# Optimization experiments

Hardware: AMD Instinct MI355X
Metric: run time of the kernel (lower is better)

## Reference

```python
import jax, jax.numpy as jnp
import numpy as np

D_MODEL = 2048
D_INNER = 4096
D_XB = 1024
D_STATE = 16
D_CONV = 4
DT_RANK = 128
BATCH = 2
SEQLEN = 2048
N_XB_HEAD = D_XB // D_STATE      # 64
N_C_HEAD = D_INNER // D_STATE    # 256
REP = N_C_HEAD // N_XB_HEAD      # 4
P = D_INNER // N_C_HEAD          # channels per head = 16


def setup_inputs() -> dict:
    key = jax.random.key(0)
    ks = jax.random.split(key, 8)
    rnd = lambda k, shape, sc: (jax.random.normal(k, shape, dtype=jnp.float32) * sc)
    hidden_states = jax.random.normal(ks[0], (BATCH, SEQLEN, D_MODEL), dtype=jnp.float32)
    in_proj_w = rnd(ks[1], (2 * D_XB + 2 * D_INNER, D_MODEL), 0.02)
    dt_in_proj_w = rnd(ks[2], (DT_RANK, D_MODEL), 0.02)
    lim = DT_RANK ** -0.5
    dt_proj_w = jax.random.uniform(ks[3], (D_INNER, DT_RANK), minval=-lim, maxval=lim, dtype=jnp.float32)
    # dt bias init: inverse-softplus of dt sampled log-uniform in [dt_min, dt_max]
    dt = jnp.exp(jax.random.uniform(ks[4], (D_INNER,), dtype=jnp.float32)
                 * (np.log(0.1) - np.log(0.001)) + np.log(0.001))
    dt = jnp.clip(dt, 1e-4, None)
    dt_proj_b = dt + jnp.log(-jnp.expm1(-dt))
    conv_w = rnd(ks[5], (D_INNER, 1, D_CONV), 0.2)
    conv_b = rnd(ks[6], (D_INNER,), 0.1)
    # A = -exp(A_log), A_log = log(arange(1..d_state)) per channel (S4D-real init)
    A_log = jnp.log(jnp.tile(jnp.arange(1, D_STATE + 1, dtype=jnp.float32), (D_INNER, 1)))
    D = jnp.ones((D_INNER,), dtype=jnp.float32)
    out_proj_w = rnd(ks[7], (D_MODEL, D_INNER), 0.02)
    return {"hidden_states": hidden_states, "in_proj_w": in_proj_w,
            "dt_in_proj_w": dt_in_proj_w, "dt_proj_w": dt_proj_w, "dt_proj_b": dt_proj_b,
            "conv_w": conv_w, "conv_b": conv_b, "A_log": A_log, "D": D,
            "out_proj_w": out_proj_w}


def reference(hidden_states, in_proj_w, dt_in_proj_w, dt_proj_w, dt_proj_b,
              conv_w, conv_b, A_log, D, out_proj_w):
    b, l, _ = hidden_states.shape
    h, p, n = N_C_HEAD, P, D_STATE
    A = -jnp.exp(A_log)                                   # (d_inner, n)
    A_h = A.reshape(h, p, n)

    zxbc = hidden_states @ in_proj_w.T                    # (b, l, 2*d_inner + 2*d_xb)
    z, x, Bm, Cm = jnp.split(zxbc, [D_INNER, D_INNER + D_XB, D_INNER + 2 * D_XB], axis=-1)

    # repeat_kv (GQA-style head repeat) on x and B before conv
    xh = jnp.repeat(x.reshape(b, l, N_XB_HEAD, D_STATE), REP, axis=2)   # (b, l, h, dstate)
    Bh = jnp.repeat(Bm.reshape(b, l, N_XB_HEAD, n), REP, axis=2)        # (b, l, h, n)
    Ch = Cm.reshape(b, l, h, n)                                         # (b, l, h, n)

    # causal depthwise conv1d + SiLU over d_inner channels
    u = xh.reshape(b, l, D_INNER).transpose(0, 2, 1)      # (b, d_inner, l)
    u = jnp.pad(u, ((0, 0), (0, 0), (D_CONV - 1, 0)))
    u = jax.lax.conv_general_dilated(u, conv_w, (1,), 'VALID',
                                     dimension_numbers=('NCH', 'OIH', 'NCH'),
                                     feature_group_count=D_INNER)
    u = jax.nn.silu(u + conv_b[None, :, None])            # (b, d_inner, l)
    u_bld = u.transpose(0, 2, 1)                          # (b, l, d_inner)

    # dt = softplus(dt_proj(dt_in_proj(h)) + dt_bias)
    dt = jax.nn.softplus((hidden_states @ dt_in_proj_w.T) @ dt_proj_w.T + dt_proj_b)  # (b, l, d_inner)

    dt_h = dt.reshape(b, l, h, p).transpose(1, 0, 2, 3)   # (l, b, h, p)
    u_h = u_bld.reshape(b, l, h, p).transpose(1, 0, 2, 3)
    B_l = Bh.transpose(1, 0, 2, 3)                        # (l, b, h, n)
    C_l = Ch.transpose(1, 0, 2, 3)

    def step(s, inp):
        dt_t, u_t, B_t, C_t = inp                         # (b,h,p),(b,h,p),(b,h,n),(b,h,n)
        dA = jnp.exp(dt_t[..., None] * A_h)               # (b, h, p, n)
        s = dA * s + (dt_t * u_t)[..., None] * B_t[:, :, None, :]
        y_t = jnp.einsum('bhpn,bhn->bhp', s, C_t)
        return s, y_t

    s0 = jnp.zeros((b, h, p, n), dtype=hidden_states.dtype)
    _, ys = jax.lax.scan(step, s0, (dt_h, u_h, B_l, C_l))  # ys: (l, b, h, p)

    y = ys.transpose(1, 0, 2, 3).reshape(b, l, D_INNER)
    y = y + u_bld * D                                      # skip term
    y = y * jax.nn.silu(z)                                 # gate
    return y @ out_proj_w.T                                # (b, l, d_model)
```

## Files before the change

kernel.cpp:

```cpp
#include <hip/hip_runtime.h>
#include <stdint.h>

#define DM    2048
#define DI    4096
#define DXB   1024
#define NPROJ 10240
#define NPROJ2 10368
#define NPAD  10496
#define DTR   128
#define LSEQ  2048
#define NBAT  2
#define TOK   4096
#define CHUNK 64
#define NCHUNK 32
#define GC    8192

typedef unsigned short u16;
typedef unsigned short u16x4 __attribute__((ext_vector_type(4)));
typedef __bf16 bf16x8 __attribute__((ext_vector_type(8)));
typedef float  f32x4  __attribute__((ext_vector_type(4)));

__device__ __forceinline__ u16 f2bf(float f) {
  union { float f; uint32_t u; } a; a.f = f;
  uint32_t u = a.u;
  return (u16)((u + 0x7fffu + ((u >> 16) & 1u)) >> 16);
}
__device__ __forceinline__ float bf2f(u16 h) {
  union { uint32_t u; float f; } a; a.u = ((uint32_t)h) << 16; return a.f;
}
__device__ __forceinline__ u16 f2h(float f) {
  _Float16 h = (_Float16)f;
  union { _Float16 h; u16 u; } a; a.h = h; return a.u;
}
__device__ __forceinline__ float h2f(u16 u) {
  union { u16 u; _Float16 h; } a; a.u = u; return (float)a.h;
}

__device__ __forceinline__ void gl_lds16(const u16* g, u16* l) {
  __builtin_amdgcn_global_load_lds(
      (const __attribute__((address_space(1))) void*)g,
      (__attribute__((address_space(3))) void*)l,
      16, 0, 0);
}

#define FENCE() asm volatile("" ::: "memory")

__device__ __forceinline__ void wpow16(float w, float* wp) {
  wp[0] = w;            wp[1] = w * w;
  wp[2] = wp[1] * w;    wp[3] = wp[1] * wp[1];
  wp[4] = wp[3] * w;    wp[5] = wp[2] * wp[2];
  wp[6] = wp[5] * w;    wp[7] = wp[3] * wp[3];
  wp[8] = wp[7] * w;    wp[9] = wp[4] * wp[4];
  wp[10] = wp[9] * w;   wp[11] = wp[5] * wp[5];
  wp[12] = wp[11] * w;  wp[13] = wp[6] * wp[6];
  wp[14] = wp[13] * w;  wp[15] = wp[7] * wp[7];
}

#define NC0 (TOK*DM/4)
#define NC1 (NC0 + NPROJ*DM/4)
#define NC2 (NC1 + DTR*DM/4)
#define NC3 (NC2 + DI*DTR/4)
#define NC4 (NC3 + DM*DI/4)
#define NC5 (NC4 + (NPAD-NPROJ2)*DM/4)
__global__ __launch_bounds__(256)
void k_prep(const float* __restrict__ hs, const float* __restrict__ wi,
            const float* __restrict__ wdti, const float* __restrict__ wdtp,
            const float* __restrict__ wo,
            u16* __restrict__ hsb, u16* __restrict__ wib, u16* __restrict__ wdtib,
            u16* __restrict__ wdtpb, u16* __restrict__ wob) {
  int i = blockIdx.x * 256 + threadIdx.x;
  if (i >= NC4) {
    if (i < NC5) {
      ((uint64_t*)(wib + (size_t)NPROJ2 * DM))[i - NC4] = 0ull;
    }
    return;
  }
  const float* src; u16* dst; int off;
  if (i < NC0)      { src = hs;   dst = hsb;   off = i; }
  else if (i < NC1) { src = wi;   dst = wib;   off = i - NC0; }
  else if (i < NC2) { src = wdti; dst = wdtib; off = i - NC1; }
  else if (i < NC3) { src = wdtp; dst = wdtpb; off = i - NC2; }
  else              { src = wo;   dst = wob;   off = i - NC3; }
  f32x4 v = ((const f32x4*)src)[off];
  union { u16 h[4]; uint64_t q; } o;
#pragma unroll
  for (int e = 0; e < 4; ++e) o.h[e] = f2bf(v[e]);
  ((uint64_t*)dst)[off] = o.q;
}

template <int MODE, int SR, int SC>
__global__ __launch_bounds__(256)
void k_gemm(const u16* __restrict__ A, const u16* __restrict__ Bw,
            int K, float* __restrict__ o_f,
            u16* __restrict__ z_b, u16* __restrict__ x_b,
            u16* __restrict__ B_b, u16* __restrict__ C_b,
            u16* __restrict__ dtl, const float* __restrict__ bias) {
  __shared__ u16 sA[128 * 64];
  __shared__ u16 sB[128 * 64];
  const int tid = threadIdx.x;
  const int lane = tid & 63, w = tid >> 6;
  const int ln = lane & 15, qd = lane >> 4;
  const int wm = w & 1, wn = w >> 1;

  int bxr, byr;
  if (SR > 0) {
    const int flat = blockIdx.y * gridDim.x + blockIdx.x;
    const int st = flat / (SR * SC), i = flat % (SR * SC);
    const int ncg = gridDim.x / SC;
    const int rg = st / ncg, cg = st % ncg;
    byr = rg * SR + i / SC;
    bxr = cg * SC + i % SC;
  } else {
    bxr = blockIdx.x; byr = blockIdx.y;
  }
  const int m0 = byr * 128, n0 = bxr * 128;

  f32x4 acc[4][4] = {};

  int srow[4], sq[4];
#pragma unroll
  for (int it = 0; it < 4; ++it) {
    int slot = it * 256 + tid;
    srow[it] = slot >> 3;
    sq[it] = (slot & 7) ^ (srow[it] & 7);
  }
  const int ch = ln & 7;

  for (int k0 = 0; k0 < K; k0 += 64) {
#pragma unroll
    for (int it = 0; it < 4; ++it) {
      int slot = it * 256 + tid;
      gl_lds16(A  + (size_t)(m0 + srow[it]) * K + k0 + sq[it] * 8, sA + slot * 8);
      gl_lds16(Bw + (size_t)(n0 + srow[it]) * K + k0 + sq[it] * 8, sB + slot * 8);
    }
    __syncthreads();
#pragma unroll
    for (int kk = 0; kk < 64; kk += 32) {
      bf16x8 af[4], bfr[4];
      const int cbase = (kk >> 3) + qd;
#pragma unroll
      for (int i = 0; i < 4; ++i) {
        int ra = wm * 64 + i * 16 + ln;
        int rb = wn * 64 + i * 16 + ln;
        af[i]  = *reinterpret_cast<const bf16x8*>(&sA[ra * 64 + (cbase ^ ch) * 8]);
        bfr[i] = *reinterpret_cast<const bf16x8*>(&sB[rb * 64 + (cbase ^ ch) * 8]);
      }
#pragma unroll
      for (int i = 0; i < 4; ++i)
#pragma unroll
        for (int j = 0; j < 4; ++j)
          acc[i][j] = __builtin_amdgcn_mfma_f32_16x16x32_bf16(af[i], bfr[j], acc[i][j], 0, 0, 0);
    }
    __syncthreads();
  }

#pragma unroll
  for (int i = 0; i < 4; ++i)
#pragma unroll
    for (int j = 0; j < 4; ++j)
#pragma unroll
      for (int r = 0; r < 4; ++r) {
        int gm = m0 + wm * 64 + i * 16 + qd * 4 + r;
        int gn = n0 + wn * 64 + j * 16 + ln;
        float v = acc[i][j][r];
        if (MODE == 2) {
          float xx = v + bias[gn];
          float sp = (xx > 15.f) ? xx : log1pf(__expf(xx));
          dtl[(size_t)gm * DI + gn] = f2h(sp);
        } else {
          o_f[(size_t)gm * DM + gn] = v;
        }
      }
}

template <int MODE>
__global__ __launch_bounds__(512, 2)
void k_gemm8(const u16* __restrict__ A, const u16* __restrict__ Bw, int K,
             float* __restrict__ o_f,
             u16* __restrict__ z_b, u16* __restrict__ x_b,
             u16* __restrict__ B_b, u16* __restrict__ C_b,
             u16* __restrict__ dtl) {
  __shared__ u16 sm[65536];
  u16* const sA = sm;
  u16* const sB = sm + 32768;

  const int tid = threadIdx.x;
  const int lane = tid & 63, w = tid >> 6;
  const int ln = lane & 15, qd = lane >> 4;
  const int wm = w & 1, wn = w >> 1, bn = wn >> 1;

  const int flat = blockIdx.y * gridDim.x + blockIdx.x;
  const int cpx = (gridDim.x * 16) >> 3;
  const int vid = (flat & 7) * cpx + (flat >> 3);
  const int byr = vid & 15, bxr = vid >> 4;
  const int m0 = byr * 256, n0 = bxr * 256;
  const int NT = K >> 6;

  const u16* agl[2]; const u16* bgl[2]; int ldst[2];
#pragma unroll
  for (int it = 0; it < 2; ++it) {
    const int slot = it * 512 + tid;
    const int srow = slot >> 3;
    const int sxk = ((slot & 7) ^ (srow & 7)) * 8;
    agl[it] = A  + (size_t)(m0 + srow) * K + sxk;
    bgl[it] = Bw + (size_t)(n0 + srow) * K + sxk;
    ldst[it] = slot * 8;
  }
  const size_t hstep = (size_t)128 * K;

  auto stA = [&](int t, int h) {
    u16* d = sA + ((t & 1) * 2 + h) * 8192;
    const size_t go = (size_t)h * hstep + (size_t)t * 64;
#pragma unroll
    for (int it = 0; it < 2; ++it) gl_lds16(agl[it] + go, d + ldst[it]);
  };
  auto stB = [&](int t, int h) {
    u16* d = sB + ((t & 1) * 2 + h) * 8192;
    const size_t go = (size_t)h * hstep + (size_t)t * 64;
#pragma unroll
    for (int it = 0; it < 2; ++it) gl_lds16(bgl[it] + go, d + ldst[it]);
  };

  const int c0 = (qd ^ (ln & 7)) * 8;
  const int c1 = c0 ^ 32;
  const int rbase = ln * 64;

  f32x4 acc[8][4] = {};
  bf16x8 a03k0[4], a47k0[4], a03k1[4], a47k1[4], bk0[4], bk1[4];

  stB(0, 0); stB(0, 1); stA(0, 0); stA(0, 1);
  if (NT > 1) {
    stB(1, 0); stB(1, 1); stA(1, 0);
    asm volatile("s_waitcnt vmcnt(6)" ::: "memory");
  } else {
    asm volatile("s_waitcnt vmcnt(0)" ::: "memory");
  }
  FENCE(); __builtin_amdgcn_s_barrier(); FENCE();

  for (int t = 0; t < NT; ++t) {
    const int aoff = ((t & 1) * 2 + wm) * 8192 + rbase;
    const int boff = ((t & 1) * 2 + bn) * 8192 + (wn & 1) * 4096 + rbase;

#pragma unroll
    for (int i = 0; i < 4; ++i)
      a03k0[i] = *(const bf16x8*)&sA[aoff + i * 1024 + c0];
#pragma unroll
    for (int j = 0; j < 4; ++j)
      bk0[j] = *(const bf16x8*)&sB[boff + j * 1024 + c0];
    if (bn == 0) {
#pragma unroll
      for (int j = 0; j < 4; ++j)
        bk1[j] = *(const bf16x8*)&sB[boff + j * 1024 + c1];
    }
    if (t + 1 < NT) stA(t + 1, 1);
    FENCE(); __builtin_amdgcn_s_barrier();
    asm volatile("s_waitcnt lgkmcnt(0)" ::: "memory");
    __builtin_amdgcn_sched_barrier(0);
    __builtin_amdgcn_s_setprio(1);
#pragma unroll
    for (int i = 0; i < 4; ++i)
#pragma unroll
      for (int j = 0; j < 4; ++j)
        acc[i][j] = __builtin_amdgcn_mfma_f32_16x16x32_bf16(a03k0[i], bk0[j], acc[i][j], 0, 0, 0);
    __builtin_amdgcn_s_setprio(0);
    FENCE(); __builtin_amdgcn_s_barrier(); FENCE();

#pragma unroll
    for (int i = 0; i < 4; ++i)
      a47k0[i] = *(const bf16x8*)&sA[aoff + (4 + i) * 1024 + c0];
    if (bn == 1) {
#pragma unroll
      for (int j = 0; j < 4; ++j)
        bk1[j] = *(const bf16x8*)&sB[boff + j * 1024 + c1];
    }
    if (t + 2 < NT) stB(t + 2, 0);
    FENCE(); __builtin_amdgcn_s_barrier();
    asm volatile("s_waitcnt lgkmcnt(0)" ::: "memory");
    __builtin_amdgcn_sched_barrier(0);
    __builtin_amdgcn_s_setprio(1);
#pragma unroll
    for (int i = 0; i < 4; ++i)
#pragma unroll
      for (int j = 0; j < 4; ++j)
        acc[4 + i][j] = __builtin_amdgcn_mfma_f32_16x16x32_bf16(a47k0[i], bk0[j], acc[4 + i][j], 0, 0, 0);
    __builtin_amdgcn_s_setprio(0);
    FENCE(); __builtin_amdgcn_s_barrier(); FENCE();

#pragma unroll
    for (int i = 0; i < 4; ++i)
      a03k1[i] = *(const bf16x8*)&sA[aoff + i * 1024 + c1];
    if (wm == 0) {
#pragma unroll
      for (int i = 0; i < 4; ++i)
        a47k1[i] = *(const bf16x8*)&sA[aoff + (4 + i) * 1024 + c1];
    }
    if (t + 2 < NT) stB(t + 2, 1);
    FENCE(); __builtin_amdgcn_s_barrier();
    asm volatile("s_waitcnt lgkmcnt(0)" ::: "memory");
    __builtin_amdgcn_sched_barrier(0);
    __builtin_amdgcn_s_setprio(1);
#pragma unroll
    for (int i = 0; i < 4; ++i)
#pragma unroll
      for (int j = 0; j < 4; ++j)
        acc[i][j] = __builtin_amdgcn_mfma_f32_16x16x32_bf16(a03k1[i], bk1[j], acc[i][j], 0, 0, 0);
    __builtin_amdgcn_s_setprio(0);
    FENCE(); __builtin_amdgcn_s_barrier(); FENCE();

    if (wm == 1) {
#pragma unroll
      for (int i = 0; i < 4; ++i)
        a47k1[i] = *(const bf16x8*)&sA[aoff + (4 + i) * 1024 + c1];
    }
    if (t + 2 < NT) stA(t + 2, 0);
    FENCE(); __builtin_amdgcn_s_barrier();
    asm volatile("s_waitcnt lgkmcnt(0)" ::: "memory");
    __builtin_amdgcn_sched_barrier(0);
    __builtin_amdgcn_s_setprio(1);
#pragma unroll
    for (int i = 0; i < 4; ++i)
#pragma unroll
      for (int j = 0; j < 4; ++j)
        acc[4 + i][j] = __builtin_amdgcn_mfma_f32_16x16x32_bf16(a47k1[i], bk1[j], acc[4 + i][j], 0, 0, 0);
    __builtin_amdgcn_s_setprio(0);
    if (t + 2 < NT)      { asm volatile("s_waitcnt vmcnt(6)" ::: "memory"); }
    else if (t + 1 < NT) { asm volatile("s_waitcnt vmcnt(0)" ::: "memory"); }
    FENCE(); __builtin_amdgcn_s_barrier(); FENCE();
  }

  if (MODE == 0) {
    u16* ob; int ld, cc;
    if (bxr < 16)      { ob = z_b; ld = DI;  cc = 0; }
    else if (bxr < 20) { ob = x_b; ld = DXB; cc = 4096; }
    else if (bxr < 24) { ob = B_b; ld = DXB; cc = 5120; }
    else if (bxr < 40) { ob = C_b; ld = DI;  cc = 6144; }
    else               { ob = dtl; ld = DTR; cc = 10240;
                         if (wn >= 2) return;
    }
    u16* ep = sm + w * 4096;
    const int rr = lane >> 4, ck = lane & 15;
#pragma unroll
    for (int i = 0; i < 8; ++i) {
#pragma unroll
      for (int j = 0; j < 4; ++j)
#pragma unroll
        for (int r = 0; r < 4; ++r)
          ep[(qd * 4 + r) * 68 + j * 16 + ln] = f2bf(acc[i][j][r]);
#pragma unroll
      for (int p = 0; p < 4; ++p) {
        const int row = p * 4 + rr;
        u16x4 v = *(const u16x4*)&ep[row * 68 + ck * 4];
        const int gm = m0 + wm * 128 + i * 16 + row;
        const int gn = n0 + wn * 64 + ck * 4 - cc;
        *(u16x4*)&ob[(size_t)gm * ld + gn] = v;
      }
    }
  } else {
#pragma unroll
    for (int i = 0; i < 8; ++i)
#pragma unroll
      for (int j = 0; j < 4; ++j)
#pragma unroll
        for (int r = 0; r < 4; ++r) {
          int gm = m0 + wm * 128 + i * 16 + qd * 4 + r;
          int gn = n0 + wn * 64 + j * 16 + ln;
          o_f[(size_t)gm * DM + gn] = acc[i][j][r];
        }
  }
}

__global__ __launch_bounds__(256)
void k_scanA(const u16* __restrict__ dtbuf, const u16* __restrict__ x_b,
             const u16* __restrict__ B_b,
             const float* __restrict__ cw, const float* __restrict__ cb,
             float* __restrict__ Sloc, float* __restrict__ cde) {
  const int tid = threadIdx.x;
  const int gc = blockIdx.x * 256 + tid;
  const int k = blockIdx.y;
  const int b = gc >> 12, c = gc & (DI - 1);
  const int hx16 = (c >> 6) << 4;
  const int xc = hx16 + (c & 15);

  const float cw0 = cw[c * 4 + 0], cw1 = cw[c * 4 + 1];
  const float cw2 = cw[c * 4 + 2], cw3 = cw[c * 4 + 3];
  const float cbv = cb[c];

  float s[16];
#pragma unroll
  for (int n = 0; n < 16; ++n) s[n] = 0.f;
  float cdt = 0.f;
  const int l0 = k * CHUNK;
  const size_t xbase = (size_t)b * LSEQ * DXB + xc;

  float xm3 = 0.f, xm2 = 0.f, xm1 = 0.f;
  if (k > 0) {
    xm3 = bf2f(x_b[xbase + (size_t)(l0 - 3) * DXB]);
    xm2 = bf2f(x_b[xbase + (size_t)(l0 - 2) * DXB]);
    xm1 = bf2f(x_b[xbase + (size_t)(l0 - 1) * DXB]);
  }

  for (int i = 0; i < CHUNK; ++i) {
    const int l = l0 + i;
    const size_t row = (size_t)b * LSEQ + l;
    float x3 = bf2f(x_b[xbase + (size_t)l * DXB]);
    float u = cbv + cw0 * xm3 + cw1 * xm2 + cw2 * xm1 + cw3 * x3;
    xm3 = xm2; xm2 = xm1; xm1 = x3;
    u = u / (1.f + __expf(-u));

    float dtv = h2f(dtbuf[row * DI + c]);
    cdt += dtv;
    float du = dtv * u;

    float w = __expf(-dtv), wp[16];
    wpow16(w, wp);

    bf16x8 B0 = ((const bf16x8*)(B_b + row * DXB + hx16))[0];
    bf16x8 B1 = ((const bf16x8*)(B_b + row * DXB + hx16))[1];
#pragma unroll
    for (int e = 0; e < 8; ++e)
      s[e] = wp[e] * s[e] + du * (float)B0[e];
#pragma unroll
    for (int e = 0; e < 8; ++e)
      s[8 + e] = wp[8 + e] * s[8 + e] + du * (float)B1[e];
  }
  float* sl = Sloc + ((size_t)k * GC + gc) * 16;
#pragma unroll
  for (int n = 0; n < 16; ++n) sl[n] = s[n];
  cde[(size_t)k * GC + gc] = cdt;
}

__global__ __launch_bounds__(256)
void k_scan2(const float* __restrict__ cde, float* __restrict__ S) {
  const int idx = blockIdx.x * 256 + threadIdx.x;
  const int gc = idx >> 4, n = idx & 15;
  const float np1 = -(float)(n + 1);
  float s = 0.f;
  for (int k = 0; k < NCHUNK; ++k) {
    const size_t off = ((size_t)k * GC + gc) * 16 + n;
    float sl = S[off];
    S[off] = s;
    s = sl + __expf(np1 * cde[(size_t)k * GC + gc]) * s;
  }
}

__global__ __launch_bounds__(256)
void k_scanB(const u16* __restrict__ dtbuf, const u16* __restrict__ x_b,
             const u16* __restrict__ B_b, const u16* __restrict__ C_b,
             const u16* __restrict__ z_b,
             const float* __restrict__ Dp, const float* __restrict__ cw,
             const float* __restrict__ cb, const float* __restrict__ Sin,
             u16* __restrict__ yg) {
  const int tid = threadIdx.x;
  const int gc = blockIdx.x * 256 + tid;
  const int k = blockIdx.y;
  const int b = gc >> 12, c = gc & (DI - 1);
  const int hx16 = (c >> 6) << 4;
  const int h16 = (c >> 4) << 4;
  const int xc = hx16 + (c & 15);

  const float cw0 = cw[c * 4 + 0], cw1 = cw[c * 4 + 1];
  const float cw2 = cw[c * 4 + 2], cw3 = cw[c * 4 + 3];
  const float cbv = cb[c], Dv = Dp[c];

  float s[16];
  const float* sp = Sin + ((size_t)k * GC + gc) * 16;
#pragma unroll
  for (int n = 0; n < 16; ++n) s[n] = sp[n];

  const int l0 = k * CHUNK;
  const size_t xbase = (size_t)b * LSEQ * DXB + xc;

  float xm3 = 0.f, xm2 = 0.f, xm1 = 0.f;
  if (k > 0) {
    xm3 = bf2f(x_b[xbase + (size_t)(l0 - 3) * DXB]);
    xm2 = bf2f(x_b[xbase + (size_t)(l0 - 2) * DXB]);
    xm1 = bf2f(x_b[xbase + (size_t)(l0 - 1) * DXB]);
  }

  for (int i = 0; i < CHUNK; ++i) {
    const int l = l0 + i;
    const size_t row = (size_t)b * LSEQ + l;
    float x3 = bf2f(x_b[xbase + (size_t)l * DXB]);
    float u = cbv + cw0 * xm3 + cw1 * xm2 + cw2 * xm1 + cw3 * x3;
    xm3 = xm2; xm2 = xm1; xm1 = x3;
    u = u / (1.f + __expf(-u));

    float dtv = h2f(dtbuf[row * DI + c]);
    float du = dtv * u;

    float w = __expf(-dtv), wp[16];
    wpow16(w, wp);

    bf16x8 B0 = ((const bf16x8*)(B_b + row * DXB + hx16))[0];
    bf16x8 B1 = ((const bf16x8*)(B_b + row * DXB + hx16))[1];
    bf16x8 C0 = ((const bf16x8*)(C_b + row * DI + h16))[0];
    bf16x8 C1 = ((const bf16x8*)(C_b + row * DI + h16))[1];

    float y = 0.f;
#pragma unroll
    for (int e = 0; e < 8; ++e) {
      s[e] = wp[e] * s[e] + du * (float)B0[e];
      y += s[e] * (float)C0[e];
    }
#pragma unroll
    for (int e = 0; e < 8; ++e) {
      s[8 + e] = wp[8 + e] * s[8 + e] + du * (float)B1[e];
      y += s[8 + e] * (float)C1[e];
    }
    float zv = bf2f(z_b[row * DI + c]);
    float g = zv / (1.f + __expf(-zv));
    yg[row * DI + c] = f2bf((y + u * Dv) * g);
  }
}

extern "C" void kernel_launch(void* const* d_in, const int* in_sizes, int n_in,
                              void* d_out, int out_size, void* d_ws, size_t ws_size,
                              hipStream_t stream) {
  const float* hs   = (const float*)d_in[0];
  const float* wi   = (const float*)d_in[1];
  const float* wdti = (const float*)d_in[2];
  const float* wdtp = (const float*)d_in[3];
  const float* dtb  = (const float*)d_in[4];
  const float* cw   = (const float*)d_in[5];
  const float* cb   = (const float*)d_in[6];
  const float* Dp   = (const float*)d_in[8];
  const float* wo   = (const float*)d_in[9];
  float* out = (float*)d_out;

  char* p = (char*)d_ws;
  auto alloc = [&](size_t bytes) {
    char* r = p; p += (bytes + 255) & ~(size_t)255; return (void*)r;
  };
  char* R0 = (char*)alloc(64ull << 20);
  u16*   hsb   = (u16*)R0;
  u16*   wib   = (u16*)(R0 + (16ull << 20));
  u16*   wdtib = (u16*)(R0 + (56ull << 20));
  u16*   dtbuf = (u16*)R0;

  u16*   wdtpb = (u16*)alloc((size_t)DI * DTR * 2);
  u16*   wob   = (u16*)alloc((size_t)DM * DI * 2);
  u16*   z_b   = (u16*)alloc((size_t)TOK * DI * 2);
  u16*   x_b   = (u16*)alloc((size_t)TOK * DXB * 2);
  u16*   B_b   = (u16*)alloc((size_t)TOK * DXB * 2);
  u16*   C_b   = (u16*)alloc((size_t)TOK * DI * 2);
  u16*   dtlow = (u16*)alloc((size_t)TOK * DTR * 2);
  u16*   yg    = (u16*)alloc((size_t)TOK * DI * 2);
  float* Sloc  = (float*)alloc((size_t)NCHUNK * GC * 16 * 4);
  float* cde   = (float*)alloc((size_t)NCHUNK * GC * 4);

  k_prep<<<(NC5 + 255) / 256, 256, 0, stream>>>(
      hs, wi, wdti, wdtp, wo, hsb, wib, wdtib, wdtpb, wob);

  k_gemm8<0><<<dim3(NPAD / 256, TOK / 256), 512, 0, stream>>>(
      hsb, wib, DM, nullptr, z_b, x_b, B_b, C_b, dtlow);
  k_gemm<2, 0, 0><<<dim3(DI / 128, TOK / 128), 256, 0, stream>>>(
      dtlow, wdtpb, DTR, nullptr, nullptr, nullptr, nullptr, nullptr, dtbuf, dtb);

  k_scanA<<<dim3(GC / 256, NCHUNK), 256, 0, stream>>>(
      dtbuf, x_b, B_b, cw, cb, Sloc, cde);
  k_scan2<<<GC * 16 / 256, 256, 0, stream>>>(cde, Sloc);
  k_scanB<<<dim3(GC / 256, NCHUNK), 256, 0, stream>>>(
      dtbuf, x_b, B_b, C_b, z_b, Dp, cw, cb, Sloc, yg);

  k_gemm<3, 16, 16><<<dim3(DM / 128, TOK / 128), 256, 0, stream>>>(
      yg, wob, DI, out, nullptr, nullptr, nullptr, nullptr, nullptr, nullptr);
}
```

Before: 660.5 us.

## Add 8-wave 256x128 GEMM for out_proj and drop mid-phase barriers in gemm8

Replaces the 128x128 four-wave out-projection GEMM with a new 512-thread kernel that computes 256x128 tiles. It uses double-buffered LDS, direct global-to-LDS loads, split K-halves shared across waves, and a swizzled block order for better cache locality. Separately, the in_proj gemm8 kernel drops one of the two barriers per phase, relying on the lgkmcnt wait alone, which cuts synchronisation but risks LDS read/write races between waves.

```diff
diff --git a/kernel.cpp b/kernel.cpp
--- a/kernel.cpp
+++ b/kernel.cpp
@@ -253,7 +253,6 @@
         bk1[j] = *(const bf16x8*)&sB[boff + j * 1024 + c1];
     }
     if (t + 1 < NT) stA(t + 1, 1);
-    FENCE(); __builtin_amdgcn_s_barrier();
     asm volatile("s_waitcnt lgkmcnt(0)" ::: "memory");
     __builtin_amdgcn_sched_barrier(0);
     __builtin_amdgcn_s_setprio(1);
@@ -274,7 +273,6 @@
         bk1[j] = *(const bf16x8*)&sB[boff + j * 1024 + c1];
     }
     if (t + 2 < NT) stB(t + 2, 0);
-    FENCE(); __builtin_amdgcn_s_barrier();
     asm volatile("s_waitcnt lgkmcnt(0)" ::: "memory");
     __builtin_amdgcn_sched_barrier(0);
     __builtin_amdgcn_s_setprio(1);
@@ -295,7 +293,6 @@
         a47k1[i] = *(const bf16x8*)&sA[aoff + (4 + i) * 1024 + c1];
     }
     if (t + 2 < NT) stB(t + 2, 1);
-    FENCE(); __builtin_amdgcn_s_barrier();
     asm volatile("s_waitcnt lgkmcnt(0)" ::: "memory");
     __builtin_amdgcn_sched_barrier(0);
     __builtin_amdgcn_s_setprio(1);
@@ -313,7 +310,6 @@
         a47k1[i] = *(const bf16x8*)&sA[aoff + (4 + i) * 1024 + c1];
     }
     if (t + 2 < NT) stA(t + 2, 0);
-    FENCE(); __builtin_amdgcn_s_barrier();
     asm volatile("s_waitcnt lgkmcnt(0)" ::: "memory");
     __builtin_amdgcn_sched_barrier(0);
     __builtin_amdgcn_s_setprio(1);
@@ -328,7 +324,7 @@
     FENCE(); __builtin_amdgcn_s_barrier(); FENCE();
   }
 
-  if (MODE == 0) {
+  {
     u16* ob; int ld, cc;
     if (bxr < 16)      { ob = z_b; ld = DI;  cc = 0; }
     else if (bxr < 20) { ob = x_b; ld = DXB; cc = 4096; }
@@ -355,18 +351,138 @@
         *(u16x4*)&ob[(size_t)gm * ld + gn] = v;
       }
     }
+  }
+}
+
+__global__ __launch_bounds__(512, 2)
+void k_gemm8n(const u16* __restrict__ A, const u16* __restrict__ Bw, int K,
+              float* __restrict__ o_f) {
+  __shared__ u16 sm[49152];
+  u16* const sA = sm;
+  u16* const sB = sm + 32768;
+
+  const int tid = threadIdx.x;
+  const int lane = tid & 63, w = tid >> 6;
+  const int ln = lane & 15, qd = lane >> 4;
+  const int wm = w >> 1, wn = w & 1;
+  const int wmh = wm >> 1;
+
+  const int flat = blockIdx.y * gridDim.x + blockIdx.x;
+  const int cpx = (gridDim.x * 16) >> 3;
+  const int vid = (flat & 7) * cpx + (flat >> 3);
+  const int byr = vid & 15, bxr = vid >> 4;
+  const int m0 = byr * 256, n0 = bxr * 128;
+  const int NT = K >> 6;
+
+  const u16* agl[2]; int ldstA[2];
+#pragma unroll
+  for (int it = 0; it < 2; ++it) {
+    const int slot = it * 512 + tid;
+    const int srow = slot >> 3;
+    agl[it] = A + (size_t)(m0 + srow) * K + ((slot & 7) ^ (srow & 7)) * 8;
+    ldstA[it] = slot * 8;
+  }
+  const int srB = tid >> 3;
+  const u16* bgl = Bw + (size_t)(n0 + srB) * K + ((tid & 7) ^ (srB & 7)) * 8;
+  const int ldstB = tid * 8;
+  const size_t hstepA = (size_t)128 * K;
+  const size_t hstepB = (size_t)64 * K;
+
+  auto stA = [&](int t, int h) {
+    u16* d = sA + ((t & 1) * 2 + h) * 8192;
+    const size_t go = (size_t)h * hstepA + (size_t)t * 64;
+#pragma unroll
+    for (int it = 0; it < 2; ++it) gl_lds16(agl[it] + go, d + ldstA[it]);
+  };
+  auto stB = [&](int t, int h) {
+    gl_lds16(bgl + (size_t)h * hstepB + (size_t)t * 64,
+             sB + (t & 1) * 8192 + h * 4096 + ldstB);
+  };
+
+  const int c0 = (qd ^ (ln & 7)) * 8;
+  const int c1 = c0 ^ 32;
+  const int arow = ((wm & 1) * 64 + ln) * 64;
+  const int brow = ln * 64;
+
+  f32x4 acc[4][4] = {};
+  bf16x8 ak0[4], ak1[4], bk0[4], bk1[4];
+
+  stA(0, 0); stA(0, 1); stB(0, 0); stB(0, 1);
+  if (NT > 1) {
+    stA(1, 0); stB(1, 0);
+    asm volatile("s_waitcnt vmcnt(3)" ::: "memory");
   } else {
-#pragma unroll
-    for (int i = 0; i < 8; ++i)
-#pragma unroll
-      for (int j = 0; j < 4; ++j)
-#pragma unroll
-        for (int r = 0; r < 4; ++r) {
-          int gm = m0 + wm * 128 + i * 16 + qd * 4 + r;
-          int gn = n0 + wn * 64 + j * 16 + ln;
-          o_f[(size_t)gm * DM + gn] = acc[i][j][r];
-        }
-  }
+    asm volatile("s_waitcnt vmcnt(0)" ::: "memory");
+  }
+  FENCE(); __builtin_amdgcn_s_barrier(); FENCE();
+
+  for (int t = 0; t < NT; ++t) {
+    const int aoff = ((t & 1) * 2 + wmh) * 8192 + arow;
+    const int boff = (t & 1) * 8192 + wn * 4096 + brow;
+
+#pragma unroll
+    for (int i = 0; i < 4; ++i)
+      ak0[i] = *(const bf16x8*)&sA[aoff + i * 1024 + c0];
+#pragma unroll
+    for (int j = 0; j < 4; ++j)
+      bk0[j] = *(const bf16x8*)&sB[boff + j * 1024 + c0];
+    if (wmh == 0) {
+#pragma unroll
+      for (int i = 0; i < 4; ++i)
+        ak1[i] = *(const bf16x8*)&sA[aoff + i * 1024 + c1];
+    }
+    if (wn == 0) {
+#pragma unroll
+      for (int j = 0; j < 4; ++j)
+        bk1[j] = *(const bf16x8*)&sB[boff + j * 1024 + c1];
+    }
+    if (t + 1 < NT) { stA(t + 1, 1); stB(t + 1, 1); }
+    asm volatile("s_waitcnt lgkmcnt(0)" ::: "memory");
+    __builtin_amdgcn_sched_barrier(0);
+    __builtin_amdgcn_s_setprio(1);
+#pragma unroll
+    for (int i = 0; i < 4; ++i)
+#pragma unroll
+      for (int j = 0; j < 4; ++j)
+        acc[i][j] = __builtin_amdgcn_mfma_f32_16x16x32_bf16(ak0[i], bk0[j], acc[i][j], 0, 0, 0);
+    __builtin_amdgcn_s_setprio(0);
+    FENCE(); __builtin_amdgcn_s_barrier(); FENCE();
+
+    if (wmh == 1) {
+#pragma unroll
+      for (int i = 0; i < 4; ++i)
+        ak1[i] = *(const bf16x8*)&sA[aoff + i * 1024 + c1];
+    }
+    if (wn == 1) {
+#pragma unroll
+      for (int j = 0; j < 4; ++j)
+        bk1[j] = *(const bf16x8*)&sB[boff + j * 1024 + c1];
+    }
+    if (t + 2 < NT) { stA(t + 2, 0); stB(t + 2, 0); }
+    asm volatile("s_waitcnt lgkmcnt(0)" ::: "memory");
+    __builtin_amdgcn_sched_barrier(0);
+    __builtin_amdgcn_s_setprio(1);
+#pragma unroll
+    for (int i = 0; i < 4; ++i)
+#pragma unroll
+      for (int j = 0; j < 4; ++j)
+        acc[i][j] = __builtin_amdgcn_mfma_f32_16x16x32_bf16(ak1[i], bk1[j], acc[i][j], 0, 0, 0);
+    __builtin_amdgcn_s_setprio(0);
+    if (t + 2 < NT)      { asm volatile("s_waitcnt vmcnt(3)" ::: "memory"); }
+    else if (t + 1 < NT) { asm volatile("s_waitcnt vmcnt(0)" ::: "memory"); }
+    FENCE(); __builtin_amdgcn_s_barrier(); FENCE();
+  }
+
+#pragma unroll
+  for (int i = 0; i < 4; ++i)
+#pragma unroll
+    for (int j = 0; j < 4; ++j)
+#pragma unroll
+      for (int r = 0; r < 4; ++r) {
+        int gm = m0 + wm * 64 + i * 16 + qd * 4 + r;
+        int gn = n0 + wn * 64 + j * 16 + ln;
+        o_f[(size_t)gm * DM + gn] = acc[i][j][r];
+      }
 }
 
 __global__ __launch_bounds__(256)
@@ -562,6 +678,6 @@
   k_scanB<<<dim3(GC / 256, NCHUNK), 256, 0, stream>>>(
       dtbuf, x_b, B_b, C_b, z_b, Dp, cw, cb, Sloc, yg);
 
-  k_gemm<3, 16, 16><<<dim3(DM / 128, TOK / 128), 256, 0, stream>>>(
-      yg, wob, DI, out, nullptr, nullptr, nullptr, nullptr, nullptr, nullptr);
-}
+  k_gemm8n<<<dim3(DM / 128, TOK / 256), 512, 0, stream>>>(
+      yg, wob, DI, out);
+}
```

New measurement: 630.5 us. 1.05x faster.
